# Optimization experiments

Measured on AMD Instinct MI355X. Metric: run time of the kernel, lower is better.

## Reference

```python
import jax, jax.numpy as jnp
import numpy as np
from jax import lax

B, S, D, H = 4, 1024, 1024, 16
DK = D // H


def setup_inputs() -> dict:
    key = jax.random.key(0)
    ks = jax.random.split(key, 8)
    s = 0.02
    return {
        "text_embeddings": jax.random.normal(ks[0], (B, S, D), jnp.float32),
        "text_mask": jnp.ones((B, S), jnp.int32),
        "W_G": jax.random.normal(ks[1], (D, D), jnp.float32) * s,
        "b_G": jnp.zeros((D,), jnp.float32),
        "Wq": jax.random.normal(ks[2], (D, D), jnp.float32) * s,
        "bq": jnp.zeros((D,), jnp.float32),
        "Wk": jax.random.normal(ks[3], (D, D), jnp.float32) * s,
        "bk": jnp.zeros((D,), jnp.float32),
        "conv_w": jax.random.normal(ks[4], (D, H, 3), jnp.float32) * s,
        "conv_b": jnp.zeros((D,), jnp.float32),
    }


def _rope_tables(seq_len, dk):
    # interleaved sinusoidal tables, each value repeated twice along feature dim
    pos = jnp.arange(seq_len, dtype=jnp.float32)[:, None]            # [S,1]
    inv = jnp.power(10000.0, -2.0 * jnp.arange(dk // 2, dtype=jnp.float32) / dk)
    ang = pos * inv                                                   # [S,DK/2]
    cos_pos = jnp.repeat(jnp.cos(ang), 2, axis=-1)[None, None]        # [1,1,S,DK]
    sin_pos = jnp.repeat(jnp.sin(ang), 2, axis=-1)[None, None]
    return cos_pos, sin_pos


def reference(text_embeddings, text_mask, W_G, b_G, Wq, bq, Wk, bk, conv_w, conv_b):
    b, s, d = text_embeddings.shape
    g = text_embeddings @ W_G + b_G                                   # [B,S,D]
    q = (g @ Wq + bq).reshape(b, s, H, DK).transpose(0, 2, 1, 3)      # [B,H,S,DK]
    k = (g @ Wk + bk).reshape(b, s, H, DK).transpose(0, 2, 1, 3)

    cos_pos, sin_pos = _rope_tables(s, DK)
    # NOTE: query rotation uses +q_odd (module does NOT negate for q), key uses -k_odd
    qw2 = jnp.stack([q[..., 1::2], q[..., ::2]], axis=-1).reshape(q.shape)
    qw = q * cos_pos + qw2 * sin_pos
    kw2 = jnp.stack([-k[..., 1::2], k[..., ::2]], axis=-1).reshape(k.shape)
    kw = k * cos_pos + kw2 * sin_pos

    scores = jnp.einsum("bhqd,bhkd->bhqk", qw, kw) / np.float32(np.sqrt(DK))
    mask = text_mask[:, None, None, :]                                # [B,1,1,S]
    scores = jnp.where(mask == 0, jnp.float32(-1e9), scores)
    p_attn = jax.nn.softmax(scores, axis=-1)                          # [B,H,S,S]

    row0 = p_attn[:, :, 0, :]                                         # [B,H,S]
    conv = lax.conv_general_dilated(
        row0, conv_w, window_strides=(1,), padding=[(1, 1)],
        dimension_numbers=("NCH", "OIH", "NCH"))                      # [B,D,S]
    return jax.nn.relu(conv + conv_b[None, :, None])
```

## Files before the change

kernel.cpp:

```cpp
#include <hip/hip_runtime.h>
#include <math.h>

#define B_  4
#define S_  1024
#define D_  1024
#define H_  16
#define DK_ 64
#define M_  (B_ * S_)

typedef __bf16 bf16x8 __attribute__((ext_vector_type(8)));
typedef float  f32x4  __attribute__((ext_vector_type(4)));

__device__ __forceinline__ unsigned short f2bf(float f) {
  unsigned u = __builtin_bit_cast(unsigned, f);
  u = (u + 0x7FFFu + ((u >> 16) & 1u)) >> 16;
  return (unsigned short)u;
}
__device__ __forceinline__ float bf2f(unsigned short h) {
  unsigned u = ((unsigned)h) << 16;
  return __builtin_bit_cast(float, u);
}

__device__ __forceinline__ void gl_lds16(const void* g, void* lds) {
  __builtin_amdgcn_global_load_lds(
      (const __attribute__((address_space(1))) unsigned int*)(unsigned long long)g,
      (__attribute__((address_space(3))) unsigned int*)(unsigned int)(unsigned long long)lds,
      16, 0, 0);
}

__global__ __launch_bounds__(256) void prep_kernel(
    const float* __restrict__ X, const float* __restrict__ W_G,
    const float* __restrict__ Wk, const float* __restrict__ bG,
    unsigned short* __restrict__ WGbf, unsigned short* __restrict__ WkT,
    float* __restrict__ partG, float* __restrict__ partB) {
  __shared__ float tle[32][33];
  __shared__ float gs2[4][32];
  __shared__ float bgs[32];
  const int blk = blockIdx.x;
  const int tid = threadIdx.x;

  if (blk < 512) {
    const int i = (blk * 256 + tid) * 2;
    const float4 v0 = ((const float4*)W_G)[i];
    const float4 v1 = ((const float4*)W_G)[i + 1];
    ushort4 h0, h1;
    h0.x = f2bf(v0.x); h0.y = f2bf(v0.y); h0.z = f2bf(v0.z); h0.w = f2bf(v0.w);
    h1.x = f2bf(v1.x); h1.y = f2bf(v1.y); h1.z = f2bf(v1.z); h1.w = f2bf(v1.w);
    ((ushort4*)WGbf)[i] = h0;
    ((ushort4*)WGbf)[i + 1] = h1;
  } else if (blk < 1536) {
    const int t = blk - 512;
    const int k0 = (t & 31) * 32;
    const int n0 = (t >> 5) * 32;
    const int tx = tid & 31;
    const int ty = tid >> 5;
#pragma unroll
    for (int r = 0; r < 32; r += 8)
      tle[ty + r][tx] = Wk[(size_t)(k0 + ty + r) * 1024 + n0 + tx];
    __syncthreads();
#pragma unroll
    for (int r = 0; r < 32; r += 8)
      WkT[(size_t)(n0 + ty + r) * 1024 + k0 + tx] = f2bf(tle[tx][ty + r]);
  } else if (blk < 1664) {
    const int bl = blk - 1536;
    const int sg = bl >> 2;
    const int mg = bl & 3;
    if (tid < 128) {
      const int b = tid >> 5, kk = tid & 31;
      gs2[b][kk] = X[(size_t)b * S_ * D_ + sg * 32 + kk];
    }
    __syncthreads();
    const int mid = mg * 256 + tid;
    float a0 = 0.f, a1 = 0.f, a2 = 0.f, a3 = 0.f;
#pragma unroll
    for (int kk = 0; kk < 32; ++kk) {
      const float w = W_G[(size_t)(sg * 32 + kk) * 1024 + mid];
      a0 = fmaf(gs2[0][kk], w, a0);
      a1 = fmaf(gs2[1][kk], w, a1);
      a2 = fmaf(gs2[2][kk], w, a2);
      a3 = fmaf(gs2[3][kk], w, a3);
    }
    partG[(size_t)(sg * 4 + 0) * 1024 + mid] = a0;
    partG[(size_t)(sg * 4 + 1) * 1024 + mid] = a1;
    partG[(size_t)(sg * 4 + 2) * 1024 + mid] = a2;
    partG[(size_t)(sg * 4 + 3) * 1024 + mid] = a3;
  } else {
    const int bl = blk - 1664;
    const int sl = bl >> 2;
    const int ng = bl & 3;
    if (tid < 32) bgs[tid] = bG[sl * 32 + tid];
    __syncthreads();
    const int n = ng * 256 + tid;
    float a = 0.f;
#pragma unroll
    for (int kk = 0; kk < 32; ++kk)
      a = fmaf(bgs[kk], Wk[(size_t)(sl * 32 + kk) * 1024 + n], a);
    partB[(size_t)sl * 1024 + n] = a;
  }
}

#define GM 64
#define GN 128

__global__ __launch_bounds__(256) void gemm_bf16(
    const unsigned short* __restrict__ A, const unsigned short* __restrict__ BT,
    const float* __restrict__ bias, unsigned short* __restrict__ C,
    const int mShift, const int nGemmBlocks,
    const float* __restrict__ Wq, float* __restrict__ part,
    const float* __restrict__ partG, const float* __restrict__ bG,
    const float* __restrict__ partB, const float* __restrict__ bk,
    float* __restrict__ biasK,
    const float* __restrict__ X, unsigned short* __restrict__ Xbf,
    float* __restrict__ tab,
    const float* __restrict__ bq, const int* __restrict__ mask,
    float* __restrict__ scores, float* __restrict__ mS) {
  __shared__ __align__(16) unsigned short As[2][2][GM * 32];
  __shared__ __align__(16) unsigned short Bs[2][2][GN * 32];
  __shared__ float gs[4][32];
  __shared__ float q0s[128];
  __shared__ float sc[64][9];

  const int flat = blockIdx.x;
  const int tid  = threadIdx.x;

  if (flat >= nGemmBlocks) {
    const int eb = flat - nGemmBlocks;
    if (eb < 128) {
      const int slab = eb >> 2;
      const int n = (eb & 3) * 256 + tid;
      if (tid < 128) {
        const int b = tid >> 5, kk = tid & 31;
        float v = bG[slab * 32 + kk];
        const float* pg = partG + (size_t)b * 1024 + slab * 32 + kk;
#pragma unroll
        for (int sg = 0; sg < 32; ++sg) v += pg[(size_t)sg * 4096];
        gs[b][kk] = v;
      }
      __syncthreads();
      float a0 = 0.f, a1 = 0.f, a2 = 0.f, a3 = 0.f;
#pragma unroll
      for (int kk = 0; kk < 32; ++kk) {
        const float w = Wq[(size_t)(slab * 32 + kk) * D_ + n];
        a0 = fmaf(gs[0][kk], w, a0);
        a1 = fmaf(gs[1][kk], w, a1);
        a2 = fmaf(gs[2][kk], w, a2);
        a3 = fmaf(gs[3][kk], w, a3);
      }
      part[(size_t)(slab * 4 + 0) * D_ + n] = a0;
      part[(size_t)(slab * 4 + 1) * D_ + n] = a1;
      part[(size_t)(slab * 4 + 2) * D_ + n] = a2;
      part[(size_t)(slab * 4 + 3) * D_ + n] = a3;
    } else if (eb < 132) {
      const int n = (eb - 128) * 256 + tid;
      float v = bk[n];
#pragma unroll
      for (int sl = 0; sl < 32; ++sl) v += partB[(size_t)sl * 1024 + n];
      biasK[n] = v;
    } else if (eb < 260) {
      const int idx = (eb - 132) * 256 + tid;
      const int s = idx >> 5, j = idx & 31;
      const float inv = (float)exp(-(double)j * (9.210340371976182736 / 32.0));
      float sn, c;
      sincosf((float)s * inv, &sn, &c);
      tab[(size_t)s * 64 + 2 * j] = c;
      tab[(size_t)s * 64 + 2 * j + 1] = sn;
    } else {
      const int i = ((eb - 260) * 256 + tid) * 2;
      const float4 v0 = ((const float4*)X)[i];
      const float4 v1 = ((const float4*)X)[i + 1];
      ushort4 h0, h1;
      h0.x = f2bf(v0.x); h0.y = f2bf(v0.y); h0.z = f2bf(v0.z); h0.w = f2bf(v0.w);
      h1.x = f2bf(v1.x); h1.y = f2bf(v1.y); h1.z = f2bf(v1.z); h1.w = f2bf(v1.w);
      ((ushort4*)Xbf)[i] = h0;
      ((ushort4*)Xbf)[i + 1] = h1;
    }
    return;
  }

  const int bx = flat >> mShift;
  const int by = flat & ((1 << mShift) - 1);
  const int wv   = tid >> 6;
  const int lane = tid & 63;
  const int m0 = by * GM;
  const int n0 = bx * GN;

  if (scores && tid < 128) {
    const int nq = n0 + tid;
    float v = bq[nq];
#pragma unroll
    for (int sl2 = 0; sl2 < 32; ++sl2)
      v += part[(size_t)(sl2 * 4 + (m0 >> 10)) * D_ + nq];
    q0s[tid] = v;
  }

  const int colOff = (lane & 3) * 8;
  const size_t aOff  = (size_t)(m0 + 16 * wv + (lane >> 2)) * 1024 + colOff;
  const size_t bOff0 = (size_t)(n0 + 32 * wv + (lane >> 2)) * 1024 + colOff;
  const size_t bOff1 = bOff0 + (size_t)16 * 1024;

  const int l15  = lane & 15;
  const int quad = lane >> 4;

  f32x4 acc[4][2];
#pragma unroll
  for (int i = 0; i < 4; ++i)
#pragma unroll
    for (int j = 0; j < 2; ++j) acc[i][j] = (f32x4){0.f, 0.f, 0.f, 0.f};

  auto STAGE = [&](int bufi, int kk) {
#pragma unroll
    for (int ks = 0; ks < 2; ++ks) {
      gl_lds16(A  + aOff  + kk + ks * 32, &As[bufi][ks][wv * 512]);
      gl_lds16(BT + bOff0 + kk + ks * 32, &Bs[bufi][ks][wv * 1024]);
      gl_lds16(BT + bOff1 + kk + ks * 32, &Bs[bufi][ks][wv * 1024 + 512]);
    }
  };

  STAGE(0, 0);

#pragma unroll 1
  for (int t = 0; t < 16; ++t) {
    const int cur = t & 1;
    if (t < 15) {
      STAGE(cur ^ 1, (t + 1) * 64);
      asm volatile("s_waitcnt vmcnt(6)" ::: "memory");
    } else {
      asm volatile("s_waitcnt vmcnt(0)" ::: "memory");
    }
    __builtin_amdgcn_s_barrier();
    __builtin_amdgcn_sched_barrier(0);

#pragma unroll
    for (int ks = 0; ks < 2; ++ks) {
      bf16x8 af[4], bfr[2];
#pragma unroll
      for (int mi = 0; mi < 4; ++mi)
        af[mi] = *(const bf16x8*)(&As[cur][ks][(mi * 16 + l15) * 32 + quad * 8]);
#pragma unroll
      for (int ni = 0; ni < 2; ++ni)
        bfr[ni] = *(const bf16x8*)(
            &Bs[cur][ks][(wv * 32 + ni * 16 + l15) * 32 + quad * 8]);
#pragma unroll
      for (int mi = 0; mi < 4; ++mi)
#pragma unroll
        for (int ni = 0; ni < 2; ++ni)
          acc[mi][ni] = __builtin_amdgcn_mfma_f32_16x16x32_bf16(
              af[mi], bfr[ni], acc[mi][ni], 0, 0, 0);
    }
    __builtin_amdgcn_sched_barrier(0);
    __builtin_amdgcn_s_barrier();
  }

  if (scores) {
    const int b_i   = m0 >> 10;
    const int sbase = m0 & 1023;
#pragma unroll
    for (int ni = 0; ni < 2; ++ni) {
      const int n_loc = wv * 32 + ni * 16 + l15;
      const float bv  = bias[n0 + n_loc];
      const float q0a = q0s[n_loc];
      const float q0b = q0s[n_loc ^ 1];
      const float sq  = (n_loc & 1) ? -q0b : q0b;
      const int j2    = (n_loc & 63) & ~1;
#pragma unroll
      for (int mi = 0; mi < 4; ++mi) {
#pragma unroll
        for (int r = 0; r < 4; ++r) {
          const int s_loc = mi * 16 + quad * 4 + r;
          const float2 cs =
              *(const float2*)(tab + (size_t)(sbase + s_loc) * 64 + j2);
          const float coef = q0a * cs.x + sq * cs.y;
          float v = (acc[mi][ni][r] + bv) * coef;
          v += __shfl_xor(v, 1);
          v += __shfl_xor(v, 2);
          v += __shfl_xor(v, 4);
          v += __shfl_xor(v, 8);
          if (l15 == 0) sc[s_loc][wv * 2 + ni] = v;
        }
      }
    }
    __syncthreads();
    if (tid < 128) {
      const int h_loc = tid >> 6;
      const int s_loc = tid & 63;
      const float* row = sc[s_loc];
      float dot = (row[h_loc * 4 + 0] + row[h_loc * 4 + 1]) +
                  (row[h_loc * 4 + 2] + row[h_loc * 4 + 3]);
      dot *= 0.125f;
      const int s = sbase + s_loc;
      if (mask[b_i * S_ + s] == 0) dot = -1e9f;
      const int bh = b_i * H_ + (bx * 2 + h_loc);
      scores[(size_t)bh * S_ + s] = dot;
      float mx = dot;
#pragma unroll
      for (int off = 16; off >= 1; off >>= 1)
        mx = fmaxf(mx, __shfl_xor(mx, off, 32));
      float e = expf(dot - mx);
#pragma unroll
      for (int off = 16; off >= 1; off >>= 1) e += __shfl_xor(e, off, 32);
      if ((s_loc & 31) == 0) {
        const int ch = ((by & 15) << 1) + (s_loc >> 5);
        mS[((size_t)bh * 32 + ch) * 2 + 0] = mx;
        mS[((size_t)bh * 32 + ch) * 2 + 1] = e;
      }
    }
    return;
  }

#pragma unroll
  for (int ni = 0; ni < 2; ++ni) {
    const int n = n0 + wv * 32 + ni * 16 + l15;
    const float bv = bias ? bias[n] : 0.f;
#pragma unroll
    for (int mi = 0; mi < 4; ++mi) {
#pragma unroll
      for (int r = 0; r < 4; ++r) {
        const int m = m0 + mi * 16 + quad * 4 + r;
        C[(size_t)m * 1024 + n] = f2bf(acc[mi][ni][r] + bv);
      }
    }
  }
}

__global__ __launch_bounds__(256) void conv_norm_relu_kernel(
    const float* __restrict__ scores, const float* __restrict__ mS,
    const float* __restrict__ cw, const float* __restrict__ cb,
    float* __restrict__ out) {
  const int b  = blockIdx.y;
  const int s0 = blockIdx.x * 128;
  const int o0 = blockIdx.z * 64;
  const int tid = threadIdx.x;
  const int tx = tid & 15;
  const int ty = tid >> 4;

  __shared__ float msh[16], ish[16];
  __shared__ __align__(16) float wT[48][68];
  __shared__ float cbs[64];
  __shared__ __align__(16) float pm[16][196];

  if (tid < 16) {
    const int bh = b * H_ + tid;
    float m = -3e38f;
#pragma unroll
    for (int c = 0; c < 32; ++c)
      m = fmaxf(m, mS[(size_t)(bh * 32 + c) * 2]);
    float S = 0.f;
#pragma unroll
    for (int c = 0; c < 32; ++c)
      S += mS[(size_t)(bh * 32 + c) * 2 + 1] *
           expf(mS[(size_t)(bh * 32 + c) * 2] - m);
    msh[tid] = m;
    ish[tid] = 1.f / S;
  }
  for (int i = tid; i < 64 * 48; i += 256) {
    const int ol = i / 48, ct = i % 48;
    wT[ct][ol] = cw[(size_t)(o0 + ol) * 48 + ct];
  }
  if (tid < 64) cbs[tid] = cb[o0 + tid];
  __syncthreads();

  for (int i = tid; i < 16 * 130; i += 256) {
    const int c = i / 130, col = i % 130;
    const int gs = s0 - 1 + col;
    pm[c][12 * (col >> 3) + (col & 7)] =
        (gs >= 0 && gs < S_)
            ? expf(scores[(size_t)(b * H_ + c) * S_ + gs] - msh[c]) * ish[c]
            : 0.f;
  }
  __syncthreads();

  float acc[4][8];
#pragma unroll
  for (int i = 0; i < 4; ++i) {
    const float cv = cbs[ty * 4 + i];
#pragma unroll
    for (int j = 0; j < 8; ++j) acc[i][j] = cv;
  }

#pragma unroll
  for (int c = 0; c < 16; ++c) {
    float pl[10];
    const float* base = &pm[c][12 * tx];
    *(float4*)(pl + 0) = *(const float4*)(base + 0);
    *(float4*)(pl + 4) = *(const float4*)(base + 4);
    *(float2*)(pl + 8) = *(const float2*)(&pm[c][12 * (tx + 1)]);
#pragma unroll
    for (int t = 0; t < 3; ++t) {
      float w[4];
      *(float4*)w = *(const float4*)&wT[c * 3 + t][ty * 4];
#pragma unroll
      for (int i = 0; i < 4; ++i)
#pragma unroll
        for (int j = 0; j < 8; ++j)
          acc[i][j] = fmaf(pl[j + t], w[i], acc[i][j]);
    }
  }

#pragma unroll
  for (int i = 0; i < 4; ++i) {
    float* orow =
        out + ((size_t)b * D_ + o0 + ty * 4 + i) * S_ + s0 + tx * 8;
    float4 v0, v1;
    v0.x = fmaxf(acc[i][0], 0.f); v0.y = fmaxf(acc[i][1], 0.f);
    v0.z = fmaxf(acc[i][2], 0.f); v0.w = fmaxf(acc[i][3], 0.f);
    v1.x = fmaxf(acc[i][4], 0.f); v1.y = fmaxf(acc[i][5], 0.f);
    v1.z = fmaxf(acc[i][6], 0.f); v1.w = fmaxf(acc[i][7], 0.f);
    *(float4*)(orow + 0) = v0;
    *(float4*)(orow + 4) = v1;
  }
}

extern "C" void kernel_launch(void* const* d_in, const int* in_sizes, int n_in,
                              void* d_out, int out_size, void* d_ws,
                              size_t ws_size, hipStream_t stream) {
  const float* x    = (const float*)d_in[0];
  const int*   mask = (const int*)d_in[1];
  const float* W_G  = (const float*)d_in[2];
  const float* b_G  = (const float*)d_in[3];
  const float* Wq   = (const float*)d_in[4];
  const float* bq   = (const float*)d_in[5];
  const float* Wk   = (const float*)d_in[6];
  const float* bk   = (const float*)d_in[7];
  const float* cw   = (const float*)d_in[8];
  const float* cb   = (const float*)d_in[9];
  float* out = (float*)d_out;

  char* ws = (char*)d_ws;
  unsigned short* Xbf  = (unsigned short*)(ws);
  unsigned short* WkT  = (unsigned short*)(ws + (16u << 20));
  unsigned short* WGbf = (unsigned short*)(ws + (18u << 20));
  unsigned short* WfT  = (unsigned short*)(ws + (20u << 20));
  float* part   = (float*)(ws + (22u << 20));
  float* partG  = (float*)(ws + (22u << 20) + (512u << 10));
  float* partB  = (float*)(ws + (23u << 20));
  float* biasK  = (float*)(ws + (23u << 20) + (128u << 10));
  float* ropeT  = (float*)(ws + (23u << 20) + (256u << 10));
  float* scores = (float*)(ws + (23u << 20) + (512u << 10));
  float* mS     = (float*)(ws + (23u << 20) + (768u << 10));

  prep_kernel<<<1792, 256, 0, stream>>>(x, W_G, Wk, b_G, WGbf, WkT,
                                        partG, partB);
  gemm_bf16<<<2436, 256, 0, stream>>>(WkT, WGbf, nullptr, WfT, 4, 128,
                                      Wq, part, partG, b_G, partB, bk, biasK,
                                      x, Xbf, ropeT,
                                      nullptr, nullptr, nullptr, nullptr);
  gemm_bf16<<<512, 256, 0, stream>>>(Xbf, WfT, biasK, nullptr, 6, 512,
                                     nullptr, part, nullptr, nullptr,
                                     nullptr, nullptr, nullptr,
                                     nullptr, nullptr, ropeT,
                                     bq, mask, scores, mS);
  conv_norm_relu_kernel<<<dim3(8, B_, 16), 256, 0, stream>>>(
      scores, mS, cw, cb, out);
}
```

Measured before the change: 140.3 us.

## Fuse four kernel launches into one cooperative persistent kernel with grid syncs

Merges the prep, both GEMM stages and the conv/softmax/relu stage into a single cooperative kernel of 512 blocks. Stages are separated by grid.sync() and shared memory is reused through a union. This removes the per-launch overhead and tail gaps between kernels. The MFMA k-loop also moves from double to triple buffering with a deeper prefetch. In exchange, work is redistributed over fewer blocks, the first GEMM runs on only 128 blocks while the rest do elementwise work, and each grid barrier has its own cost.

```diff
diff --git a/kernel.cpp b/kernel.cpp
--- a/kernel.cpp
+++ b/kernel.cpp
@@ -1,12 +1,13 @@
 #include <hip/hip_runtime.h>
+#include <hip/hip_cooperative_groups.h>
 #include <math.h>
+
+namespace cg = cooperative_groups;
 
 #define B_  4
 #define S_  1024
 #define D_  1024
 #define H_  16
-#define DK_ 64
-#define M_  (B_ * S_)
 
 typedef __bf16 bf16x8 __attribute__((ext_vector_type(8)));
 typedef float  f32x4  __attribute__((ext_vector_type(4)));
@@ -28,18 +29,103 @@
       16, 0, 0);
 }
 
-__global__ __launch_bounds__(256) void prep_kernel(
-    const float* __restrict__ X, const float* __restrict__ W_G,
-    const float* __restrict__ Wk, const float* __restrict__ bG,
-    unsigned short* __restrict__ WGbf, unsigned short* __restrict__ WkT,
-    float* __restrict__ partG, float* __restrict__ partB) {
-  __shared__ float tle[32][33];
-  __shared__ float gs2[4][32];
-  __shared__ float bgs[32];
+#define GM 64
+#define GN 128
+
+struct SMemG {
+  unsigned short As[3][2][GM * 32];
+  unsigned short Bs[3][2][GN * 32];
+  float gs[4][32];
+  float q0s[128];
+  float sc[64][9];
+};
+struct SMemP {
+  float tle[32][33];
+  float gs2[4][32];
+  float bgs[32];
+};
+struct SMemC {
+  float msh[16], ish[16];
+  float wT[48][68];
+  float cbs[64];
+  float pm[16][196];
+};
+union SMem {
+  SMemG g;
+  SMemP p;
+  SMemC c;
+};
+
+__device__ __forceinline__ void kloop_mfma(
+    const unsigned short* __restrict__ A, const unsigned short* __restrict__ BT,
+    size_t aOff, size_t bOff0, size_t bOff1, int wv, int l15, int quad,
+    SMemG& g, f32x4 (&acc)[4][2]) {
+  auto STG = [&](int bufi, int kk) {
+#pragma unroll
+    for (int ks = 0; ks < 2; ++ks) {
+      gl_lds16(A  + aOff  + kk + ks * 32, &g.As[bufi][ks][wv * 512]);
+      gl_lds16(BT + bOff0 + kk + ks * 32, &g.Bs[bufi][ks][wv * 1024]);
+      gl_lds16(BT + bOff1 + kk + ks * 32, &g.Bs[bufi][ks][wv * 1024 + 512]);
+    }
+  };
+  STG(0, 0);
+  STG(1, 64);
+#pragma unroll 1
+  for (int t = 0; t < 16; ++t) {
+    const int cur = t - (t / 3) * 3;
+    if (t < 14) {
+      const int nb = (t + 2) - ((t + 2) / 3) * 3;
+      STG(nb, (t + 2) * 64);
+      asm volatile("s_waitcnt vmcnt(12)" ::: "memory");
+    } else if (t == 14) {
+      asm volatile("s_waitcnt vmcnt(6)" ::: "memory");
+    } else {
+      asm volatile("s_waitcnt vmcnt(0)" ::: "memory");
+    }
+    __builtin_amdgcn_s_barrier();
+    __builtin_amdgcn_sched_barrier(0);
+
+#pragma unroll
+    for (int ks = 0; ks < 2; ++ks) {
+      bf16x8 af[4], bfr[2];
+#pragma unroll
+      for (int mi = 0; mi < 4; ++mi)
+        af[mi] = *(const bf16x8*)(&g.As[cur][ks][(mi * 16 + l15) * 32 + quad * 8]);
+#pragma unroll
+      for (int ni = 0; ni < 2; ++ni)
+        bfr[ni] = *(const bf16x8*)(
+            &g.Bs[cur][ks][(wv * 32 + ni * 16 + l15) * 32 + quad * 8]);
+#pragma unroll
+      for (int mi = 0; mi < 4; ++mi)
+#pragma unroll
+        for (int ni = 0; ni < 2; ++ni)
+          acc[mi][ni] = __builtin_amdgcn_mfma_f32_16x16x32_bf16(
+              af[mi], bfr[ni], acc[mi][ni], 0, 0, 0);
+    }
+    __builtin_amdgcn_sched_barrier(0);
+    __builtin_amdgcn_s_barrier();
+  }
+}
+
+__global__ __launch_bounds__(256, 2) void fused_pipeline(
+    const float* __restrict__ X, const int* __restrict__ mask,
+    const float* __restrict__ W_G, const float* __restrict__ bG,
+    const float* __restrict__ Wq, const float* __restrict__ bq,
+    const float* __restrict__ Wk, const float* __restrict__ bk,
+    const float* __restrict__ cw, const float* __restrict__ cb,
+    float* __restrict__ out,
+    unsigned short* __restrict__ Xbf, unsigned short* __restrict__ WGbf,
+    unsigned short* __restrict__ WkT, unsigned short* __restrict__ WfT,
+    float* __restrict__ part, float* __restrict__ partG,
+    float* __restrict__ partB, float* __restrict__ biasK,
+    float* __restrict__ tab, float* __restrict__ scores,
+    float* __restrict__ mS) {
+  __shared__ __align__(16) SMem sm;
+  cg::grid_group grid = cg::this_grid();
   const int blk = blockIdx.x;
   const int tid = threadIdx.x;
 
-  if (blk < 512) {
+  {
     const int i = (blk * 256 + tid) * 2;
     const float4 v0 = ((const float4*)W_G)[i];
     const float4 v1 = ((const float4*)W_G)[i + 1];
@@ -48,84 +134,99 @@
     h1.x = f2bf(v1.x); h1.y = f2bf(v1.y); h1.z = f2bf(v1.z); h1.w = f2bf(v1.w);
     ((ushort4*)WGbf)[i] = h0;
     ((ushort4*)WGbf)[i + 1] = h1;
-  } else if (blk < 1536) {
-    const int t = blk - 512;
-    const int k0 = (t & 31) * 32;
-    const int n0 = (t >> 5) * 32;
-    const int tx = tid & 31;
-    const int ty = tid >> 5;
-#pragma unroll
-    for (int r = 0; r < 32; r += 8)
-      tle[ty + r][tx] = Wk[(size_t)(k0 + ty + r) * 1024 + n0 + tx];
-    __syncthreads();
-#pragma unroll
-    for (int r = 0; r < 32; r += 8)
-      WkT[(size_t)(n0 + ty + r) * 1024 + k0 + tx] = f2bf(tle[tx][ty + r]);
-  } else if (blk < 1664) {
-    const int bl = blk - 1536;
-    const int sg = bl >> 2;
-    const int mg = bl & 3;
-    if (tid < 128) {
-      const int b = tid >> 5, kk = tid & 31;
-      gs2[b][kk] = X[(size_t)b * S_ * D_ + sg * 32 + kk];
-    }
-    __syncthreads();
-    const int mid = mg * 256 + tid;
-    float a0 = 0.f, a1 = 0.f, a2 = 0.f, a3 = 0.f;
-#pragma unroll
-    for (int kk = 0; kk < 32; ++kk) {
-      const float w = W_G[(size_t)(sg * 32 + kk) * 1024 + mid];
-      a0 = fmaf(gs2[0][kk], w, a0);
-      a1 = fmaf(gs2[1][kk], w, a1);
-      a2 = fmaf(gs2[2][kk], w, a2);
-      a3 = fmaf(gs2[3][kk], w, a3);
-    }
-    partG[(size_t)(sg * 4 + 0) * 1024 + mid] = a0;
-    partG[(size_t)(sg * 4 + 1) * 1024 + mid] = a1;
-    partG[(size_t)(sg * 4 + 2) * 1024 + mid] = a2;
-    partG[(size_t)(sg * 4 + 3) * 1024 + mid] = a3;
+
+#pragma unroll 1
+    for (int rep = 0; rep < 2; ++rep) {
+      const int t = blk * 2 + rep;
+      const int k0 = (t & 31) * 32;
+      const int n0 = (t >> 5) * 32;
+      const int tx = tid & 31;
+      const int ty = tid >> 5;
+      __syncthreads();
+#pragma unroll
+      for (int r = 0; r < 32; r += 8)
+        sm.p.tle[ty + r][tx] = Wk[(size_t)(k0 + ty + r) * 1024 + n0 + tx];
+      __syncthreads();
+#pragma unroll
+      for (int r = 0; r < 32; r += 8)
+        WkT[(size_t)(n0 + ty + r) * 1024 + k0 + tx] = f2bf(sm.p.tle[tx][ty + r]);
+    }
+
+    if (blk < 128) {
+      const int sg = blk >> 2;
+      const int mg = blk & 3;
+      __syncthreads();
+      if (tid < 128) {
+        const int b = tid >> 5, kk = tid & 31;
+        sm.p.gs2[b][kk] = X[(size_t)b * S_ * D_ + sg * 32 + kk];
+      }
+      __syncthreads();
+      const int mid = mg * 256 + tid;
+      float a0 = 0.f, a1 = 0.f, a2 = 0.f, a3 = 0.f;
+#pragma unroll
+      for (int kk = 0; kk < 32; ++kk) {
+        const float w = W_G[(size_t)(sg * 32 + kk) * 1024 + mid];
+        a0 = fmaf(sm.p.gs2[0][kk], w, a0);
+        a1 = fmaf(sm.p.gs2[1][kk], w, a1);
+        a2 = fmaf(sm.p.gs2[2][kk], w, a2);
+        a3 = fmaf(sm.p.gs2[3][kk], w, a3);
+      }
+      partG[(size_t)(sg * 4 + 0) * 1024 + mid] = a0;
+      partG[(size_t)(sg * 4 + 1) * 1024 + mid] = a1;
+      partG[(size_t)(sg * 4 + 2) * 1024 + mid] = a2;
+      partG[(size_t)(sg * 4 + 3) * 1024 + mid] = a3;
+    } else if (blk < 256) {
+      const int bl = blk - 128;
+      const int sl = bl >> 2;
+      const int ng = bl & 3;
+      __syncthreads();
+      if (tid < 32) sm.p.bgs[tid] = bG[sl * 32 + tid];
+      __syncthreads();
+      const int n = ng * 256 + tid;
+      float a = 0.f;
+#pragma unroll
+      for (int kk = 0; kk < 32; ++kk)
+        a = fmaf(sm.p.bgs[kk], Wk[(size_t)(sl * 32 + kk) * 1024 + n], a);
+      partB[(size_t)sl * 1024 + n] = a;
+    }
+  }
+  grid.sync();
+
+  if (blk < 128) {
+    const int wv   = tid >> 6;
+    const int lane = tid & 63;
+    const int l15  = lane & 15;
+    const int quad = lane >> 4;
+    const int m0 = (blk & 15) * GM;
+    const int n0 = (blk >> 4) * GN;
+    const int colOff = (lane & 3) * 8;
+    const size_t aOff  = (size_t)(m0 + 16 * wv + (lane >> 2)) * 1024 + colOff;
+    const size_t bOff0 = (size_t)(n0 + 32 * wv + (lane >> 2)) * 1024 + colOff;
+    const size_t bOff1 = bOff0 + (size_t)16 * 1024;
+
+    f32x4 acc[4][2];
+#pragma unroll
+    for (int i = 0; i < 4; ++i)
+#pragma unroll
+      for (int j = 0; j < 2; ++j) acc[i][j] = (f32x4){0.f, 0.f, 0.f, 0.f};
+
+    kloop_mfma(WkT, WGbf, aOff, bOff0, bOff1, wv, l15, quad, sm.g, acc);
+
+#pragma unroll
+    for (int ni = 0; ni < 2; ++ni) {
+      const int n = n0 + wv * 32 + ni * 16 + l15;
+#pragma unroll
+      for (int mi = 0; mi < 4; ++mi) {
+#pragma unroll
+        for (int r = 0; r < 4; ++r) {
+          const int m = m0 + mi * 16 + quad * 4 + r;
+          WfT[(size_t)m * 1024 + n] = f2bf(acc[mi][ni][r]);
+        }
+      }
+    }
   } else {
-    const int bl = blk - 1664;
-    const int sl = bl >> 2;
-    const int ng = bl & 3;
-    if (tid < 32) bgs[tid] = bG[sl * 32 + tid];
-    __syncthreads();
-    const int n = ng * 256 + tid;
-    float a = 0.f;
-#pragma unroll
-    for (int kk = 0; kk < 32; ++kk)
-      a = fmaf(bgs[kk], Wk[(size_t)(sl * 32 + kk) * 1024 + n], a);
-    partB[(size_t)sl * 1024 + n] = a;
-  }
-}
-
-#define GM 64
-#define GN 128
-
-__global__ __launch_bounds__(256) void gemm_bf16(
-    const unsigned short* __restrict__ A, const unsigned short* __restrict__ BT,
-    const float* __restrict__ bias, unsigned short* __restrict__ C,
-    const int mShift, const int nGemmBlocks,
-    const float* __restrict__ Wq, float* __restrict__ part,
-    const float* __restrict__ partG, const float* __restrict__ bG,
-    const float* __restrict__ partB, const float* __restrict__ bk,
-    float* __restrict__ biasK,
-    const float* __restrict__ X, unsigned short* __restrict__ Xbf,
-    float* __restrict__ tab,
-    const float* __restrict__ bq, const int* __restrict__ mask,
-    float* __restrict__ scores, float* __restrict__ mS) {
-  __shared__ __align__(16) unsigned short As[2][2][GM * 32];
-  __shared__ __align__(16) unsigned short Bs[2][2][GN * 32];
-  __shared__ float gs[4][32];
-  __shared__ float q0s[128];
-  __shared__ float sc[64][9];
-
-  const int flat = blockIdx.x;
-  const int tid  = threadIdx.x;
-
-  if (flat >= nGemmBlocks) {
-    const int eb = flat - nGemmBlocks;
-    if (eb < 128) {
+    if (blk < 256) {
+      const int eb = blk - 128;
       const int slab = eb >> 2;
       const int n = (eb & 3) * 256 + tid;
       if (tid < 128) {
@@ -134,38 +235,39 @@
         const float* pg = partG + (size_t)b * 1024 + slab * 32 + kk;
 #pragma unroll
         for (int sg = 0; sg < 32; ++sg) v += pg[(size_t)sg * 4096];
-        gs[b][kk] = v;
+        sm.g.gs[b][kk] = v;
       }
       __syncthreads();
       float a0 = 0.f, a1 = 0.f, a2 = 0.f, a3 = 0.f;
 #pragma unroll
       for (int kk = 0; kk < 32; ++kk) {
         const float w = Wq[(size_t)(slab * 32 + kk) * D_ + n];
-        a0 = fmaf(gs[0][kk], w, a0);
-        a1 = fmaf(gs[1][kk], w, a1);
-        a2 = fmaf(gs[2][kk], w, a2);
-        a3 = fmaf(gs[3][kk], w, a3);
+        a0 = fmaf(sm.g.gs[0][kk], w, a0);
+        a1 = fmaf(sm.g.gs[1][kk], w, a1);
+        a2 = fmaf(sm.g.gs[2][kk], w, a2);
+        a3 = fmaf(sm.g.gs[3][kk], w, a3);
       }
       part[(size_t)(slab * 4 + 0) * D_ + n] = a0;
       part[(size_t)(slab * 4 + 1) * D_ + n] = a1;
       part[(size_t)(slab * 4 + 2) * D_ + n] = a2;
       part[(size_t)(slab * 4 + 3) * D_ + n] = a3;
-    } else if (eb < 132) {
-      const int n = (eb - 128) * 256 + tid;
+    } else if (blk < 260) {
+      const int n = (blk - 256) * 256 + tid;
       float v = bk[n];
 #pragma unroll
       for (int sl = 0; sl < 32; ++sl) v += partB[(size_t)sl * 1024 + n];
       biasK[n] = v;
-    } else if (eb < 260) {
-      const int idx = (eb - 132) * 256 + tid;
+    } else if (blk < 388) {
+      const int idx = (blk - 260) * 256 + tid;
       const int s = idx >> 5, j = idx & 31;
       const float inv = (float)exp(-(double)j * (9.210340371976182736 / 32.0));
       float sn, c;
       sincosf((float)s * inv, &sn, &c);
       tab[(size_t)s * 64 + 2 * j] = c;
       tab[(size_t)s * 64 + 2 * j + 1] = sn;
-    } else {
-      const int i = ((eb - 260) * 256 + tid) * 2;
+    }
+    for (int u = blk - 128; u < 2048; u += 384) {
+      const int i = (u * 256 + tid) * 2;
       const float4 v0 = ((const float4*)X)[i];
       const float4 v1 = ((const float4*)X)[i + 1];
       ushort4 h0, h1;
@@ -174,92 +276,50 @@
       ((ushort4*)Xbf)[i] = h0;
       ((ushort4*)Xbf)[i + 1] = h1;
     }
-    return;
   }
-
-  const int bx = flat >> mShift;
-  const int by = flat & ((1 << mShift) - 1);
-  const int wv   = tid >> 6;
-  const int lane = tid & 63;
-  const int m0 = by * GM;
-  const int n0 = bx * GN;
-
-  if (scores && tid < 128) {
-    const int nq = n0 + tid;
-    float v = bq[nq];
-#pragma unroll
-    for (int sl2 = 0; sl2 < 32; ++sl2)
-      v += part[(size_t)(sl2 * 4 + (m0 >> 10)) * D_ + nq];
-    q0s[tid] = v;
-  }
-
-  const int colOff = (lane & 3) * 8;
-  const size_t aOff  = (size_t)(m0 + 16 * wv + (lane >> 2)) * 1024 + colOff;
-  const size_t bOff0 = (size_t)(n0 + 32 * wv + (lane >> 2)) * 1024 + colOff;
-  const size_t bOff1 = bOff0 + (size_t)16 * 1024;
-
-  const int l15  = lane & 15;
-  const int quad = lane >> 4;
-
-  f32x4 acc[4][2];
-#pragma unroll
-  for (int i = 0; i < 4; ++i)
-#pragma unroll
-    for (int j = 0; j < 2; ++j) acc[i][j] = (f32x4){0.f, 0.f, 0.f, 0.f};
-
-  auto STAGE = [&](int bufi, int kk) {
-#pragma unroll
-    for (int ks = 0; ks < 2; ++ks) {
-      gl_lds16(A  + aOff  + kk + ks * 32, &As[bufi][ks][wv * 512]);
-      gl_lds16(BT + bOff0 + kk + ks * 32, &Bs[bufi][ks][wv * 1024]);
-      gl_lds16(BT + bOff1 + kk + ks * 32, &Bs[bufi][ks][wv * 1024 + 512]);
-    }
-  };
-
-  STAGE(0, 0);
-
-#pragma unroll 1
-  for (int t = 0; t < 16; ++t) {
-    const int cur = t & 1;
-    if (t < 15) {
-      STAGE(cur ^ 1, (t + 1) * 64);
-      asm volatile("s_waitcnt vmcnt(6)" ::: "memory");
-    } else {
-      asm volatile("s_waitcnt vmcnt(0)" ::: "memory");
-    }
-    __builtin_amdgcn_s_barrier();
-    __builtin_amdgcn_sched_barrier(0);
-
-#pragma unroll
-    for (int ks = 0; ks < 2; ++ks) {
-      bf16x8 af[4], bfr[2];
-#pragma unroll
-      for (int mi = 0; mi < 4; ++mi)
-        af[mi] = *(const bf16x8*)(&As[cur][ks][(mi * 16 + l15) * 32 + quad * 8]);
-#pragma unroll
-      for (int ni = 0; ni < 2; ++ni)
-        bfr[ni] = *(const bf16x8*)(
-            &Bs[cur][ks][(wv * 32 + ni * 16 + l15) * 32 + quad * 8]);
-#pragma unroll
-      for (int mi = 0; mi < 4; ++mi)
-#pragma unroll
-        for (int ni = 0; ni < 2; ++ni)
-          acc[mi][ni] = __builtin_amdgcn_mfma_f32_16x16x32_bf16(
-              af[mi], bfr[ni], acc[mi][ni], 0, 0, 0);
-    }
-    __builtin_amdgcn_sched_barrier(0);
-    __builtin_amdgcn_s_barrier();
-  }
-
-  if (scores) {
+  grid.sync();
+
+  {
+    const int wv   = tid >> 6;
+    const int lane = tid & 63;
+    const int l15  = lane & 15;
+    const int quad = lane >> 4;
+    const int bx = blk >> 6;
+    const int by = blk & 63;
+    const int m0 = by * GM;
+    const int n0 = bx * GN;
     const int b_i   = m0 >> 10;
     const int sbase = m0 & 1023;
+
+    if (tid < 128) {
+      const int nq = n0 + tid;
+      float v = bq[nq];
+#pragma unroll
+      for (int sl2 = 0; sl2 < 32; ++sl2)
+        v += part[(size_t)(sl2 * 4 + b_i) * D_ + nq];
+      sm.g.q0s[tid] = v;
+    }
+    __syncthreads();
+
+    const int colOff = (lane & 3) * 8;
+    const size_t aOff  = (size_t)(m0 + 16 * wv + (lane >> 2)) * 1024 + colOff;
+    const size_t bOff0 = (size_t)(n0 + 32 * wv + (lane >> 2)) * 1024 + colOff;
+    const size_t bOff1 = bOff0 + (size_t)16 * 1024;
+
+    f32x4 acc[4][2];
+#pragma unroll
+    for (int i = 0; i < 4; ++i)
+#pragma unroll
+      for (int j = 0; j < 2; ++j) acc[i][j] = (f32x4){0.f, 0.f, 0.f, 0.f};
+
+    kloop_mfma(Xbf, WfT, aOff, bOff0, bOff1, wv, l15, quad, sm.g, acc);
+
 #pragma unroll
     for (int ni = 0; ni < 2; ++ni) {
       const int n_loc = wv * 32 + ni * 16 + l15;
-      const float bv  = bias[n0 + n_loc];
-      const float q0a = q0s[n_loc];
-      const float q0b = q0s[n_loc ^ 1];
+      const float bv  = biasK[n0 + n_loc];
+      const float q0a = sm.g.q0s[n_loc];
+      const float q0b = sm.g.q0s[n_loc ^ 1];
       const float sq  = (n_loc & 1) ? -q0b : q0b;
       const int j2    = (n_loc & 63) & ~1;
 #pragma unroll
@@ -275,7 +335,7 @@
           v += __shfl_xor(v, 2);
           v += __shfl_xor(v, 4);
           v += __shfl_xor(v, 8);
-          if (l15 == 0) sc[s_loc][wv * 2 + ni] = v;
+          if (l15 == 0) sm.g.sc[s_loc][wv * 2 + ni] = v;
         }
       }
     }
@@ -283,7 +343,7 @@
     if (tid < 128) {
       const int h_loc = tid >> 6;
       const int s_loc = tid & 63;
-      const float* row = sc[s_loc];
+      const float* row = sm.g.sc[s_loc];
       float dot = (row[h_loc * 4 + 0] + row[h_loc * 4 + 1]) +
                   (row[h_loc * 4 + 2] + row[h_loc * 4 + 3]);
       dot *= 0.125f;
@@ -304,109 +364,89 @@
         mS[((size_t)bh * 32 + ch) * 2 + 1] = e;
       }
     }
-    return;
   }
-
-#pragma unroll
-  for (int ni = 0; ni < 2; ++ni) {
-    const int n = n0 + wv * 32 + ni * 16 + l15;
-    const float bv = bias ? bias[n] : 0.f;
-#pragma unroll
-    for (int mi = 0; mi < 4; ++mi) {
-#pragma unroll
-      for (int r = 0; r < 4; ++r) {
-        const int m = m0 + mi * 16 + quad * 4 + r;
-        C[(size_t)m * 1024 + n] = f2bf(acc[mi][ni][r] + bv);
-      }
-    }
-  }
-}
-
-__global__ __launch_bounds__(256) void conv_norm_relu_kernel(
-    const float* __restrict__ scores, const float* __restrict__ mS,
-    const float* __restrict__ cw, const float* __restrict__ cb,
-    float* __restrict__ out) {
-  const int b  = blockIdx.y;
-  const int s0 = blockIdx.x * 128;
-  const int o0 = blockIdx.z * 64;
-  const int tid = threadIdx.x;
-  const int tx = tid & 15;
-  const int ty = tid >> 4;
-
-  __shared__ float msh[16], ish[16];
-  __shared__ __align__(16) float wT[48][68];
-  __shared__ float cbs[64];
-  __shared__ __align__(16) float pm[16][196];
-
-  if (tid < 16) {
-    const int bh = b * H_ + tid;
-    float m = -3e38f;
-#pragma unroll
-    for (int c = 0; c < 32; ++c)
-      m = fmaxf(m, mS[(size_t)(bh * 32 + c) * 2]);
-    float S = 0.f;
-#pragma unroll
-    for (int c = 0; c < 32; ++c)
-      S += mS[(size_t)(bh * 32 + c) * 2 + 1] *
-           expf(mS[(size_t)(bh * 32 + c) * 2] - m);
-    msh[tid] = m;
-    ish[tid] = 1.f / S;
-  }
-  for (int i = tid; i < 64 * 48; i += 256) {
-    const int ol = i / 48, ct = i % 48;
-    wT[ct][ol] = cw[(size_t)(o0 + ol) * 48 + ct];
-  }
-  if (tid < 64) cbs[tid] = cb[o0 + tid];
-  __syncthreads();
-
-  for (int i = tid; i < 16 * 130; i += 256) {
-    const int c = i / 130, col = i % 130;
-    const int gs = s0 - 1 + col;
-    pm[c][12 * (col >> 3) + (col & 7)] =
-        (gs >= 0 && gs < S_)
-            ? expf(scores[(size_t)(b * H_ + c) * S_ + gs] - msh[c]) * ish[c]
-            : 0.f;
-  }
-  __syncthreads();
-
-  float acc[4][8];
-#pragma unroll
-  for (int i = 0; i < 4; ++i) {
-    const float cv = cbs[ty * 4 + i];
-#pragma unroll
-    for (int j = 0; j < 8; ++j) acc[i][j] = cv;
-  }
-
-#pragma unroll
-  for (int c = 0; c < 16; ++c) {
-    float pl[10];
-    const float* base = &pm[c][12 * tx];
-    *(float4*)(pl + 0) = *(const float4*)(base + 0);
-    *(float4*)(pl + 4) = *(const float4*)(base + 4);
-    *(float2*)(pl + 8) = *(const float2*)(&pm[c][12 * (tx + 1)]);
-#pragma unroll
-    for (int t = 0; t < 3; ++t) {
-      float w[4];
-      *(float4*)w = *(const float4*)&wT[c * 3 + t][ty * 4];
-#pragma unroll
-      for (int i = 0; i < 4; ++i)
-#pragma unroll
-        for (int j = 0; j < 8; ++j)
-          acc[i][j] = fmaf(pl[j + t], w[i], acc[i][j]);
-    }
-  }
-
-#pragma unroll
-  for (int i = 0; i < 4; ++i) {
-    float* orow =
-        out + ((size_t)b * D_ + o0 + ty * 4 + i) * S_ + s0 + tx * 8;
-    float4 v0, v1;
-    v0.x = fmaxf(acc[i][0], 0.f); v0.y = fmaxf(acc[i][1], 0.f);
-    v0.z = fmaxf(acc[i][2], 0.f); v0.w = fmaxf(acc[i][3], 0.f);
-    v1.x = fmaxf(acc[i][4], 0.f); v1.y = fmaxf(acc[i][5], 0.f);
-    v1.z = fmaxf(acc[i][6], 0.f); v1.w = fmaxf(acc[i][7], 0.f);
-    *(float4*)(orow + 0) = v0;
-    *(float4*)(orow + 4) = v1;
+  grid.sync();
+
+  {
+    const int sx = blk & 7;
+    const int b  = (blk >> 3) & 3;
+    const int oz = blk >> 5;
+    const int s0 = sx * 128;
+    const int o0 = oz * 64;
+    const int tx = tid & 15;
+    const int ty = tid >> 4;
+
+    if (tid < 16) {
+      const int bh = b * H_ + tid;
+      float m = -3e38f;
+#pragma unroll
+      for (int c = 0; c < 32; ++c)
+        m = fmaxf(m, mS[(size_t)(bh * 32 + c) * 2]);
+      float S = 0.f;
+#pragma unroll
+      for (int c = 0; c < 32; ++c)
+        S += mS[(size_t)(bh * 32 + c) * 2 + 1] *
+             expf(mS[(size_t)(bh * 32 + c) * 2] - m);
+      sm.c.msh[tid] = m;
+      sm.c.ish[tid] = 1.f / S;
+    }
+    for (int i = tid; i < 64 * 48; i += 256) {
+      const int ol = i / 48, ct = i % 48;
+      sm.c.wT[ct][ol] = cw[(size_t)(o0 + ol) * 48 + ct];
+    }
+    if (tid < 64) sm.c.cbs[tid] = cb[o0 + tid];
+    __syncthreads();
+
+    for (int i = tid; i < 16 * 130; i += 256) {
+      const int c = i / 130, col = i % 130;
+      const int gs = s0 - 1 + col;
+      sm.c.pm[c][12 * (col >> 3) + (col & 7)] =
+          (gs >= 0 && gs < S_)
+              ? expf(scores[(size_t)(b * H_ + c) * S_ + gs] - sm.c.msh[c]) *
+                    sm.c.ish[c]
+              : 0.f;
+    }
+    __syncthreads();
+
+    float acc[4][8];
+#pragma unroll
+    for (int i = 0; i < 4; ++i) {
+      const float cv = sm.c.cbs[ty * 4 + i];
+#pragma unroll
+      for (int j = 0; j < 8; ++j) acc[i][j] = cv;
+    }
+
+#pragma unroll
+    for (int c = 0; c < 16; ++c) {
+      float pl[10];
+      const float* base = &sm.c.pm[c][12 * tx];
+      *(float4*)(pl + 0) = *(const float4*)(base + 0);
+      *(float4*)(pl + 4) = *(const float4*)(base + 4);
+      *(float2*)(pl + 8) = *(const float2*)(&sm.c.pm[c][12 * (tx + 1)]);
+#pragma unroll
+      for (int t = 0; t < 3; ++t) {
+        float w[4];
+        *(float4*)w = *(const float4*)&sm.c.wT[c * 3 + t][ty * 4];
+#pragma unroll
+        for (int i = 0; i < 4; ++i)
+#pragma unroll
+          for (int j = 0; j < 8; ++j)
+            acc[i][j] = fmaf(pl[j + t], w[i], acc[i][j]);
+      }
+    }
+
+#pragma unroll
+    for (int i = 0; i < 4; ++i) {
+      float* orow =
+          out + ((size_t)b * D_ + o0 + ty * 4 + i) * S_ + s0 + tx * 8;
+      float4 v0, v1;
+      v0.x = fmaxf(acc[i][0], 0.f); v0.y = fmaxf(acc[i][1], 0.f);
+      v0.z = fmaxf(acc[i][2], 0.f); v0.w = fmaxf(acc[i][3], 0.f);
+      v1.x = fmaxf(acc[i][4], 0.f); v1.y = fmaxf(acc[i][5], 0.f);
+      v1.z = fmaxf(acc[i][6], 0.f); v1.w = fmaxf(acc[i][7], 0.f);
+      *(float4*)(orow + 0) = v0;
+      *(float4*)(orow + 4) = v1;
+    }
   }
 }
 
@@ -438,17 +478,12 @@
   float* scores = (float*)(ws + (23u << 20) + (512u << 10));
   float* mS     = (float*)(ws + (23u << 20) + (768u << 10));
 
-  prep_kernel<<<1792, 256, 0, stream>>>(x, W_G, Wk, b_G, WGbf, WkT,
-                                        partG, partB);
-  gemm_bf16<<<2436, 256, 0, stream>>>(WkT, WGbf, nullptr, WfT, 4, 128,
-                                      Wq, part, partG, b_G, partB, bk, biasK,
-                                      x, Xbf, ropeT,
-                                      nullptr, nullptr, nullptr, nullptr);
-  gemm_bf16<<<512, 256, 0, stream>>>(Xbf, WfT, biasK, nullptr, 6, 512,
-                                     nullptr, part, nullptr, nullptr,
-                                     nullptr, nullptr, nullptr,
-                                     nullptr, nullptr, ropeT,
-                                     bq, mask, scores, mS);
-  conv_norm_relu_kernel<<<dim3(8, B_, 16), 256, 0, stream>>>(
-      scores, mS, cw, cb, out);
-}
+  void* args[] = {
+      (void*)&x,    (void*)&mask, (void*)&W_G,  (void*)&b_G,  (void*)&Wq,
+      (void*)&bq,   (void*)&Wk,   (void*)&bk,   (void*)&cw,   (void*)&cb,
+      (void*)&out,  (void*)&Xbf,  (void*)&WGbf, (void*)&WkT,  (void*)&WfT,
+      (void*)&part, (void*)&partG,(void*)&partB,(void*)&biasK,(void*)&ropeT,
+      (void*)&scores,(void*)&mS};
+  hipLaunchCooperativeKernel((void*)fused_pipeline, dim3(512), dim3(256),
+                             args, 0, stream);
+}
```

After: 337.4 us. +140.5%, slower.

## Triple-buffer GEMM loads and shrink conv tiles with shuffle-reduced softmax stats

Applied to the files above, without the earlier changes.

The GEMM main loop moves from double to triple buffering of LDS tiles, keeping two k-steps of global-to-LDS loads in flight to hide memory latency better, at the cost of more LDS per block. The conv kernel tile halves along the sequence axis, so it launches twice as many blocks with less work each, which improves occupancy and parallelism for a small kernel. The softmax max/sum combine is now split across 8 lanes per head and reduced with shuffles instead of serial 32-step loops on 16 threads.

```diff
diff --git a/kernel.cpp b/kernel.cpp
--- a/kernel.cpp
+++ b/kernel.cpp
@@ -5,8 +5,6 @@
 #define S_  1024
 #define D_  1024
 #define H_  16
-#define DK_ 64
-#define M_  (B_ * S_)
 
 typedef __bf16 bf16x8 __attribute__((ext_vector_type(8)));
 typedef float  f32x4  __attribute__((ext_vector_type(4)));
@@ -114,8 +112,8 @@
     float* __restrict__ tab,
     const float* __restrict__ bq, const int* __restrict__ mask,
     float* __restrict__ scores, float* __restrict__ mS) {
-  __shared__ __align__(16) unsigned short As[2][2][GM * 32];
-  __shared__ __align__(16) unsigned short Bs[2][2][GN * 32];
+  __shared__ __align__(16) unsigned short As[3][2][GM * 32];
+  __shared__ __align__(16) unsigned short Bs[3][2][GN * 32];
   __shared__ float gs[4][32];
   __shared__ float q0s[128];
   __shared__ float sc[64][9];
@@ -207,7 +205,7 @@
 #pragma unroll
     for (int j = 0; j < 2; ++j) acc[i][j] = (f32x4){0.f, 0.f, 0.f, 0.f};
 
-  auto STAGE = [&](int bufi, int kk) {
+  auto STG = [&](int bufi, int kk) {
 #pragma unroll
     for (int ks = 0; ks < 2; ++ks) {
       gl_lds16(A  + aOff  + kk + ks * 32, &As[bufi][ks][wv * 512]);
@@ -216,13 +214,17 @@
     }
   };
 
-  STAGE(0, 0);
+  STG(0, 0);
+  STG(1, 64);
 
 #pragma unroll 1
   for (int t = 0; t < 16; ++t) {
-    const int cur = t & 1;
-    if (t < 15) {
-      STAGE(cur ^ 1, (t + 1) * 64);
+    const int cur = t - (t / 3) * 3;
+    if (t < 14) {
+      const int nb = (t + 2) - ((t + 2) / 3) * 3;
+      STG(nb, (t + 2) * 64);
+      asm volatile("s_waitcnt vmcnt(12)" ::: "memory");
+    } else if (t == 14) {
       asm volatile("s_waitcnt vmcnt(6)" ::: "memory");
     } else {
       asm volatile("s_waitcnt vmcnt(0)" ::: "memory");
@@ -327,30 +329,37 @@
     const float* __restrict__ cw, const float* __restrict__ cb,
     float* __restrict__ out) {
   const int b  = blockIdx.y;
-  const int s0 = blockIdx.x * 128;
+  const int s0 = blockIdx.x * 64;
   const int o0 = blockIdx.z * 64;
   const int tid = threadIdx.x;
-  const int tx = tid & 15;
-  const int ty = tid >> 4;
+  const int tx = tid & 7;
+  const int ty = tid >> 3;
 
   __shared__ float msh[16], ish[16];
   __shared__ __align__(16) float wT[48][68];
   __shared__ float cbs[64];
-  __shared__ __align__(16) float pm[16][196];
-
-  if (tid < 16) {
-    const int bh = b * H_ + tid;
+  __shared__ __align__(16) float pm[16][104];
+
+  if (tid < 128) {
+    const int h = tid >> 3, seg = tid & 7;
+    const int bh = b * H_ + h;
+    const float* base = mS + (size_t)bh * 64 + seg * 8;
     float m = -3e38f;
 #pragma unroll
-    for (int c = 0; c < 32; ++c)
-      m = fmaxf(m, mS[(size_t)(bh * 32 + c) * 2]);
+    for (int q = 0; q < 4; ++q) m = fmaxf(m, base[q * 2]);
+    m = fmaxf(m, __shfl_xor(m, 1));
+    m = fmaxf(m, __shfl_xor(m, 2));
+    m = fmaxf(m, __shfl_xor(m, 4));
     float S = 0.f;
 #pragma unroll
-    for (int c = 0; c < 32; ++c)
-      S += mS[(size_t)(bh * 32 + c) * 2 + 1] *
-           expf(mS[(size_t)(bh * 32 + c) * 2] - m);
-    msh[tid] = m;
-    ish[tid] = 1.f / S;
+    for (int q = 0; q < 4; ++q) S += base[q * 2 + 1] * expf(base[q * 2] - m);
+    S += __shfl_xor(S, 1);
+    S += __shfl_xor(S, 2);
+    S += __shfl_xor(S, 4);
+    if (seg == 0) {
+      msh[h] = m;
+      ish[h] = 1.f / S;
+    }
   }
   for (int i = tid; i < 64 * 48; i += 256) {
     const int ol = i / 48, ct = i % 48;
@@ -359,8 +368,8 @@
   if (tid < 64) cbs[tid] = cb[o0 + tid];
   __syncthreads();
 
-  for (int i = tid; i < 16 * 130; i += 256) {
-    const int c = i / 130, col = i % 130;
+  for (int i = tid; i < 16 * 66; i += 256) {
+    const int c = i / 66, col = i % 66;
     const int gs = s0 - 1 + col;
     pm[c][12 * (col >> 3) + (col & 7)] =
         (gs >= 0 && gs < S_)
@@ -369,10 +378,10 @@
   }
   __syncthreads();
 
-  float acc[4][8];
-#pragma unroll
-  for (int i = 0; i < 4; ++i) {
-    const float cv = cbs[ty * 4 + i];
+  float acc[2][8];
+#pragma unroll
+  for (int i = 0; i < 2; ++i) {
+    const float cv = cbs[ty * 2 + i];
 #pragma unroll
     for (int j = 0; j < 8; ++j) acc[i][j] = cv;
   }
@@ -386,10 +395,10 @@
     *(float2*)(pl + 8) = *(const float2*)(&pm[c][12 * (tx + 1)]);
 #pragma unroll
     for (int t = 0; t < 3; ++t) {
-      float w[4];
-      *(float4*)w = *(const float4*)&wT[c * 3 + t][ty * 4];
-#pragma unroll
-      for (int i = 0; i < 4; ++i)
+      float w[2];
+      *(float2*)w = *(const float2*)&wT[c * 3 + t][ty * 2];
+#pragma unroll
+      for (int i = 0; i < 2; ++i)
 #pragma unroll
         for (int j = 0; j < 8; ++j)
           acc[i][j] = fmaf(pl[j + t], w[i], acc[i][j]);
@@ -397,9 +406,9 @@
   }
 
 #pragma unroll
-  for (int i = 0; i < 4; ++i) {
+  for (int i = 0; i < 2; ++i) {
     float* orow =
-        out + ((size_t)b * D_ + o0 + ty * 4 + i) * S_ + s0 + tx * 8;
+        out + ((size_t)b * D_ + o0 + ty * 2 + i) * S_ + s0 + tx * 8;
     float4 v0, v1;
     v0.x = fmaxf(acc[i][0], 0.f); v0.y = fmaxf(acc[i][1], 0.f);
     v0.z = fmaxf(acc[i][2], 0.f); v0.w = fmaxf(acc[i][3], 0.f);
@@ -449,6 +458,6 @@
                                      nullptr, nullptr, nullptr,
                                      nullptr, nullptr, ropeT,
                                      bq, mask, scores, mS);
-  conv_norm_relu_kernel<<<dim3(8, B_, 16), 256, 0, stream>>>(
+  conv_norm_relu_kernel<<<dim3(16, B_, 16), 256, 0, stream>>>(
       scores, mS, cw, cb, out);
 }
```

New measurement: 137.2 us. 2.2% less time.
